# Kernel tuning notes

Hardware: AMD Instinct MI355X
Metric: run time of the kernel (lower is better)

## Reference

```python
import jax, jax.numpy as jnp
from jax import lax
import numpy as np

UNITS = 128
IN_DIM = 512
BATCH = 128
SEQ = 1024


def setup_inputs() -> dict:
    key = jax.random.key(0)
    k1, k2, k3 = jax.random.split(key, 3)
    x = jax.random.normal(k1, (BATCH, SEQ, IN_DIM), dtype=jnp.float32)
    # glorot-ish scaling for stability
    W = jax.random.normal(k2, (IN_DIM, 4 * UNITS), dtype=jnp.float32) * (1.0 / np.sqrt(IN_DIM))
    U = jax.random.normal(k3, (UNITS, 4 * UNITS), dtype=jnp.float32) * (1.0 / np.sqrt(UNITS))
    b = jnp.zeros((4 * UNITS,), dtype=jnp.float32)
    return {"x": x, "W": W, "U": U, "b": b}


def reference(x, W, U, b):
    # Keras LSTM with activation='tanh' AND recurrent_activation='tanh'
    # (all four gates use tanh, unlike the standard sigmoid gates).
    # Gate order in Keras kernels: i, f, g(cell candidate), o.
    B = x.shape[0]
    units = U.shape[0]
    # Precompute input projections for all timesteps: [T, B, 4*units]
    xW = jnp.einsum('bti,ij->tbj', x, W) + b

    def step(carry, xw_t):
        h, c = carry
        z = xw_t + h @ U  # [B, 4*units]
        i, f, g, o = jnp.split(z, 4, axis=-1)
        i = jnp.tanh(i)
        f = jnp.tanh(f)
        g = jnp.tanh(g)
        o = jnp.tanh(o)
        c_new = f * c + i * g
        h_new = o * jnp.tanh(c_new)
        return (h_new, c_new), None

    h0 = jnp.zeros((B, units), dtype=x.dtype)
    c0 = jnp.zeros((B, units), dtype=x.dtype)
    (h_last, _), _ = lax.scan(step, (h0, c0), xW)
    return h_last  # [B, units] (return_sequences=False)
```

## Files before the change

### kernel.cpp

```cpp
#include <hip/hip_runtime.h>
#include <hip/hip_bf16.h>


#define UNITS 128
#define IN_DIM 512
#define BATCH 128
#define SEQ 1024
#define GATES 512
#define M_ROWS (BATCH * SEQ)

typedef __attribute__((ext_vector_type(8))) short short8;
typedef __attribute__((ext_vector_type(4))) float floatx4;

__device__ __forceinline__ unsigned short f2bf(float f) {
    unsigned int x = __builtin_bit_cast(unsigned int, f);
    unsigned int r = (x + 0x7fffu + ((x >> 16) & 1u)) >> 16;
    return (unsigned short)r;
}
__device__ __forceinline__ float bf2f(unsigned short u) {
    unsigned int x = ((unsigned int)u) << 16;
    return __builtin_bit_cast(float, x);
}
__device__ __forceinline__ unsigned int pack2(float lo, float hi) {
    return (unsigned int)f2bf(lo) | ((unsigned int)f2bf(hi) << 16);
}

__device__ __forceinline__ float fast_tanh(float x) {
    float xc = fminf(12.0f, fmaxf(-12.0f, x));
    float e = __expf(2.0f * xc);
    return 1.0f - 2.0f * __builtin_amdgcn_rcpf(e + 1.0f);
}

__global__ void k_wt(const float* __restrict__ W, unsigned short* __restrict__ Wt) {
    int idx = blockIdx.x * 256 + threadIdx.x;
    int n = idx >> 9;
    int k = idx & 511;
    Wt[idx] = f2bf(W[k * 512 + n]);
}

template <bool XWF32>
__global__ void __launch_bounds__(256, 2)
k_gemm(const float* __restrict__ A, const unsigned short* __restrict__ Bt,
       void* __restrict__ Cout) {
    __shared__ __align__(16) unsigned short As[128 * 40];
    __shared__ __align__(16) unsigned short Bs[128 * 40];
    const int tid = threadIdx.x;
    const int m0 = blockIdx.y << 7;
    const int n0 = blockIdx.x << 7;
    const int l = tid & 63;
    const int w = tid >> 6;
    const int wr = (w >> 1) << 6;
    const int wc = (w & 1) << 6;
    const int lrow = l & 15;
    const int lq = l >> 4;

    floatx4 acc[4][4] = {};

    const int srow = tid >> 1;
    const int soff = (tid & 1) << 4;
    const float* ap = A + (size_t)(m0 + srow) * 512 + soff;
    const unsigned short* bp = Bt + (size_t)(n0 + srow) * 512 + soff;
    unsigned short* as = &As[srow * 40 + soff];
    unsigned short* bs = &Bs[srow * 40 + soff];

    for (int k0 = 0; k0 < 512; k0 += 32) {
        float4 a0 = *(const float4*)(ap + k0);
        float4 a1 = *(const float4*)(ap + k0 + 4);
        float4 a2 = *(const float4*)(ap + k0 + 8);
        float4 a3 = *(const float4*)(ap + k0 + 12);
        uint4 b0 = *(const uint4*)(bp + k0);
        uint4 b1 = *(const uint4*)(bp + k0 + 8);
        __syncthreads();
        uint4 pa0, pa1;
        pa0.x = pack2(a0.x, a0.y); pa0.y = pack2(a0.z, a0.w);
        pa0.z = pack2(a1.x, a1.y); pa0.w = pack2(a1.z, a1.w);
        pa1.x = pack2(a2.x, a2.y); pa1.y = pack2(a2.z, a2.w);
        pa1.z = pack2(a3.x, a3.y); pa1.w = pack2(a3.z, a3.w);
        *(uint4*)as = pa0;
        *(uint4*)(as + 8) = pa1;
        *(uint4*)bs = b0;
        *(uint4*)(bs + 8) = b1;
        __syncthreads();
        short8 af[4], bfv[4];
#pragma unroll
        for (int mi = 0; mi < 4; ++mi)
            af[mi] = *(const short8*)&As[(wr + mi * 16 + lrow) * 40 + lq * 8];
#pragma unroll
        for (int ni = 0; ni < 4; ++ni)
            bfv[ni] = *(const short8*)&Bs[(wc + ni * 16 + lrow) * 40 + lq * 8];
#pragma unroll
        for (int mi = 0; mi < 4; ++mi)
#pragma unroll
            for (int ni = 0; ni < 4; ++ni)
                acc[mi][ni] = __builtin_amdgcn_mfma_f32_16x16x32_bf16(
                    af[mi], bfv[ni], acc[mi][ni], 0, 0, 0);
    }
#pragma unroll
    for (int mi = 0; mi < 4; ++mi) {
#pragma unroll
        for (int ni = 0; ni < 4; ++ni) {
            int row = m0 + wr + mi * 16 + lq * 4;
            int col = n0 + wc + ni * 16 + lrow;
            if (XWF32) {
                float* Cf = (float*)Cout;
#pragma unroll
                for (int r = 0; r < 4; ++r)
                    Cf[(size_t)(row + r) * 512 + col] = acc[mi][ni][r];
            } else {
                unsigned short* Cb = (unsigned short*)Cout;
#pragma unroll
                for (int r = 0; r < 4; ++r)
                    Cb[(size_t)(row + r) * 512 + col] = f2bf(acc[mi][ni][r]);
            }
        }
    }
}

template <bool XWF32>
__global__ void __launch_bounds__(512, 2)
k_scan(const void* __restrict__ xwv, const float* __restrict__ U,
       const float* __restrict__ bias, float* __restrict__ out) {
    __shared__ __align__(16) float h_lds[UNITS];
    __shared__ float g_lds[GATES];
    const int j = threadIdx.x;
    const int bb = blockIdx.x;

    float u_reg[128];
#pragma unroll
    for (int k = 0; k < 128; ++k) u_reg[k] = U[k * 512 + j];
    const float bj = bias[j];
    if (j < UNITS) h_lds[j] = 0.0f;
    float c = 0.0f;
    __syncthreads();

    const float* xwf = (const float*)xwv + (size_t)bb * SEQ * 512 + j;
    const unsigned short* xwb = (const unsigned short*)xwv + (size_t)bb * SEQ * 512 + j;

    float xw_cur = XWF32 ? xwf[0] : bf2f(xwb[0]);
    for (int t = 0; t < SEQ; ++t) {
        float xw_next = 0.0f;
        if (t + 1 < SEQ)
            xw_next = XWF32 ? xwf[(size_t)(t + 1) * 512] : bf2f(xwb[(size_t)(t + 1) * 512]);

        float acc0 = 0.0f, acc1 = 0.0f;
        const float4* h4 = (const float4*)h_lds;
#pragma unroll
        for (int k4 = 0; k4 < 32; ++k4) {
            float4 hv = h4[k4];
            acc0 = fmaf(hv.x, u_reg[4 * k4 + 0], acc0);
            acc1 = fmaf(hv.y, u_reg[4 * k4 + 1], acc1);
            acc0 = fmaf(hv.z, u_reg[4 * k4 + 2], acc0);
            acc1 = fmaf(hv.w, u_reg[4 * k4 + 3], acc1);
        }
        float z = xw_cur + bj + (acc0 + acc1);
        g_lds[j] = fast_tanh(z);
        __syncthreads();
        if (j < UNITS) {
            float gi = g_lds[j];
            float gf = g_lds[128 + j];
            float gg = g_lds[256 + j];
            float go = g_lds[384 + j];
            c = fmaf(gf, c, gi * gg);
            h_lds[j] = go * fast_tanh(c);
        }
        __syncthreads();
        xw_cur = xw_next;
    }
    if (j < UNITS) out[bb * UNITS + j] = h_lds[j];
}

extern "C" void kernel_launch(void* const* d_in, const int* in_sizes, int n_in,
                              void* d_out, int out_size, void* d_ws, size_t ws_size,
                              hipStream_t stream) {
    const float* x = (const float*)d_in[0];
    const float* W = (const float*)d_in[1];
    const float* U = (const float*)d_in[2];
    const float* b = (const float*)d_in[3];
    float* out = (float*)d_out;

    char* ws = (char*)d_ws;
    const size_t WT_BYTES = (size_t)512 * 512 * 2;
    unsigned short* Wt = (unsigned short*)ws;
    void* xw = (void*)(ws + WT_BYTES);
    const size_t XW_F32_BYTES = (size_t)M_ROWS * 512 * 4;
    const bool f32path = (ws_size >= WT_BYTES + XW_F32_BYTES);

    k_wt<<<dim3(1024), dim3(256), 0, stream>>>(W, Wt);

    dim3 ggrid(4, 1024);
    if (f32path) {
        k_gemm<true><<<ggrid, dim3(256), 0, stream>>>(x, Wt, xw);
        k_scan<true><<<dim3(128), dim3(512), 0, stream>>>(xw, U, b, out);
    } else {
        k_gemm<false><<<ggrid, dim3(256), 0, stream>>>(x, Wt, xw);
        k_scan<false><<<dim3(128), dim3(512), 0, stream>>>(xw, U, b, out);
    }
}
```

Measured before the change: 1.279 ms.

## Split recurrent matvec across 4-lane groups with shuffle reduction and double-buffered h

Reorganizes the scan kernel so each group of four lanes owns one hidden unit: each lane computes partial dot products for all four gates over a 32-element slice of h, and the partials are combined with xor shuffles. Every lane then has the full gate values locally, so the second barrier and the gate staging buffer go away. h is double-buffered in padded shared memory so one barrier per step is enough. Every lane now evaluates tanh redundantly, and the bias/xw value is routed into a single partial sum via selects.

```diff
diff --git a/kernel.cpp b/kernel.cpp
--- a/kernel.cpp
+++ b/kernel.cpp
@@ -120,53 +120,88 @@
 __global__ void __launch_bounds__(512, 2)
 k_scan(const void* __restrict__ xwv, const float* __restrict__ U,
        const float* __restrict__ bias, float* __restrict__ out) {
-    __shared__ __align__(16) float h_lds[UNITS];
-    __shared__ float g_lds[GATES];
+    __shared__ __align__(16) float hbuf[2 * 160];
     const int j = threadIdx.x;
     const int bb = blockIdx.x;
-
-    float u_reg[128];
-#pragma unroll
-    for (int k = 0; k < 128; ++k) u_reg[k] = U[k * 512 + j];
-    const float bj = bias[j];
-    if (j < UNITS) h_lds[j] = 0.0f;
-    float c = 0.0f;
+    const int m = j >> 2;
+    const int r = j & 3;
+
+    float u0[32], u1[32], u2[32], u3[32];
+#pragma unroll
+    for (int kk = 0; kk < 32; ++kk) {
+        const float* Up = U + (size_t)(r * 32 + kk) * 512 + m;
+        u0[kk] = Up[0];
+        u1[kk] = Up[128];
+        u2[kk] = Up[256];
+        u3[kk] = Up[384];
+    }
+    const float bj = bias[r * 128 + m];
+
+    if (j < 160) hbuf[j] = 0.0f;
     __syncthreads();
 
-    const float* xwf = (const float*)xwv + (size_t)bb * SEQ * 512 + j;
-    const unsigned short* xwb = (const unsigned short*)xwv + (size_t)bb * SEQ * 512 + j;
-
+    const float* xwf = (const float*)xwv + (size_t)bb * SEQ * 512 + r * 128 + m;
+    const unsigned short* xwb =
+        (const unsigned short*)xwv + (size_t)bb * SEQ * 512 + r * 128 + m;
+
+    float c = 0.0f, hval = 0.0f;
     float xw_cur = XWF32 ? xwf[0] : bf2f(xwb[0]);
     for (int t = 0; t < SEQ; ++t) {
         float xw_next = 0.0f;
         if (t + 1 < SEQ)
-            xw_next = XWF32 ? xwf[(size_t)(t + 1) * 512] : bf2f(xwb[(size_t)(t + 1) * 512]);
-
-        float acc0 = 0.0f, acc1 = 0.0f;
-        const float4* h4 = (const float4*)h_lds;
-#pragma unroll
-        for (int k4 = 0; k4 < 32; ++k4) {
-            float4 hv = h4[k4];
-            acc0 = fmaf(hv.x, u_reg[4 * k4 + 0], acc0);
-            acc1 = fmaf(hv.y, u_reg[4 * k4 + 1], acc1);
-            acc0 = fmaf(hv.z, u_reg[4 * k4 + 2], acc0);
-            acc1 = fmaf(hv.w, u_reg[4 * k4 + 3], acc1);
+            xw_next = XWF32 ? xwf[(size_t)(t + 1) * 512]
+                            : bf2f(xwb[(size_t)(t + 1) * 512]);
+
+        const float xb = xw_cur + bj;
+        float a0 = (r == 0) ? xb : 0.0f;
+        float a1 = (r == 1) ? xb : 0.0f;
+        float a2 = (r == 2) ? xb : 0.0f;
+        float a3 = (r == 3) ? xb : 0.0f;
+
+        const float4* h4 =
+            (const float4*)(hbuf + (t & 1) * 160 + r * 40);
+#pragma unroll
+        for (int i = 0; i < 8; ++i) {
+            float4 hv = h4[i];
+            a0 = fmaf(hv.x, u0[4 * i + 0], a0);
+            a1 = fmaf(hv.x, u1[4 * i + 0], a1);
+            a2 = fmaf(hv.x, u2[4 * i + 0], a2);
+            a3 = fmaf(hv.x, u3[4 * i + 0], a3);
+            a0 = fmaf(hv.y, u0[4 * i + 1], a0);
+            a1 = fmaf(hv.y, u1[4 * i + 1], a1);
+            a2 = fmaf(hv.y, u2[4 * i + 1], a2);
+            a3 = fmaf(hv.y, u3[4 * i + 1], a3);
+            a0 = fmaf(hv.z, u0[4 * i + 2], a0);
+            a1 = fmaf(hv.z, u1[4 * i + 2], a1);
+            a2 = fmaf(hv.z, u2[4 * i + 2], a2);
+            a3 = fmaf(hv.z, u3[4 * i + 2], a3);
+            a0 = fmaf(hv.w, u0[4 * i + 3], a0);
+            a1 = fmaf(hv.w, u1[4 * i + 3], a1);
+            a2 = fmaf(hv.w, u2[4 * i + 3], a2);
+            a3 = fmaf(hv.w, u3[4 * i + 3], a3);
         }
-        float z = xw_cur + bj + (acc0 + acc1);
-        g_lds[j] = fast_tanh(z);
-        __syncthreads();
-        if (j < UNITS) {
-            float gi = g_lds[j];
-            float gf = g_lds[128 + j];
-            float gg = g_lds[256 + j];
-            float go = g_lds[384 + j];
-            c = fmaf(gf, c, gi * gg);
-            h_lds[j] = go * fast_tanh(c);
-        }
+        a0 += __shfl_xor(a0, 1);
+        a1 += __shfl_xor(a1, 1);
+        a2 += __shfl_xor(a2, 1);
+        a3 += __shfl_xor(a3, 1);
+        a0 += __shfl_xor(a0, 2);
+        a1 += __shfl_xor(a1, 2);
+        a2 += __shfl_xor(a2, 2);
+        a3 += __shfl_xor(a3, 2);
+
+        const float gi = fast_tanh(a0);
+        const float gf = fast_tanh(a1);
+        const float gg = fast_tanh(a2);
+        const float go = fast_tanh(a3);
+        c = fmaf(gf, c, gi * gg);
+        hval = go * fast_tanh(c);
+
+        if (r == 0)
+            hbuf[((t + 1) & 1) * 160 + (m >> 5) * 40 + (m & 31)] = hval;
         __syncthreads();
         xw_cur = xw_next;
     }
-    if (j < UNITS) out[bb * UNITS + j] = h_lds[j];
+    if (r == 0) out[bb * UNITS + m] = hval;
 }
 
 extern "C" void kernel_launch(void* const* d_in, const int* in_sizes, int n_in,
```

New measurement: 1.217 ms. -4.8%, faster.
